# Kernel optimization log

Hardware: AMD Instinct MI355X
Metric: run time of the kernel (lower is better)

The kernel has to match this reference:

```python
import jax, jax.numpy as jnp
import numpy as np

THRESHOLD = 0.5


def setup_inputs() -> dict:
    key = jax.random.key(0)
    T, B = 2048, 4096
    x = jax.random.uniform(key, (T, B, 2), dtype=jnp.float32)  # push/pop signals in [0,1]
    state0 = jnp.zeros((B, 2), dtype=jnp.float32)  # [count, tanh(count)]
    return {"x": x, "state0": state0}


def _step(state, xt):
    # state: [B, 2] = [count, tanh(count)]; xt: [B, 2] = [push, pop]
    push_sig = xt[..., 0]
    pop_sig = xt[..., 1]
    is_push = (push_sig >= THRESHOLD) & (push_sig >= pop_sig)
    is_pop = (pop_sig >= THRESHOLD) & (pop_sig > push_sig)
    delta = jnp.where(is_push, 1.0, jnp.where(is_pop, -1.0, 0.0))
    count = state[..., 0] + delta
    new_state = jnp.stack([count, jnp.tanh(count)], axis=-1)
    return new_state, new_state


def reference(x, state0):
    # x: [T, B, 2], state0: [B, 2] -> all per-step states [T, B, 2]
    _, states = jax.lax.scan(_step, state0, x)
    return states
```

## Files before the change

kernel.cpp:

```cpp
#include <hip/hip_runtime.h>
#include <math.h>

#define T_TOTAL 2048
#define B_TOTAL 4096
#define NCHUNK  32
#define TCHUNK  (T_TOTAL / NCHUNK)

__device__ __forceinline__ int delta_of(float p, float q) {
    return (p >= 0.5f && p >= q) ? 1 : ((q >= 0.5f && q > p) ? -1 : 0);
}

__global__ void scan_pass1(const float* __restrict__ x, int* __restrict__ partial) {
    const int b = blockIdx.x * blockDim.x + threadIdx.x;
    const int c = blockIdx.y;
    const float2* __restrict__ x2 = (const float2*)x;
    const int t0 = c * TCHUNK;
    int sum = 0;
#pragma unroll 4
    for (int t = t0; t < t0 + TCHUNK; ++t) {
        float2 v = x2[(size_t)t * B_TOTAL + b];
        sum += delta_of(v.x, v.y);
    }
    partial[c * B_TOTAL + b] = sum;
}

__global__ void scan_pass2(int* __restrict__ partial) {
    const int b = blockIdx.x * blockDim.x + threadIdx.x;
    int off = 0;
#pragma unroll
    for (int c = 0; c < NCHUNK; ++c) {
        int v = partial[c * B_TOTAL + b];
        partial[c * B_TOTAL + b] = off;
        off += v;
    }
}

__global__ void scan_pass3(const float* __restrict__ x, const int* __restrict__ partial,
                           float* __restrict__ out) {
    const int b = blockIdx.x * blockDim.x + threadIdx.x;
    const int c = blockIdx.y;
    const float2* __restrict__ x2 = (const float2*)x;
    float2* __restrict__ o2 = (float2*)out;
    const int t0 = c * TCHUNK;
    int count = partial[c * B_TOTAL + b];
#pragma unroll 4
    for (int t = t0; t < t0 + TCHUNK; ++t) {
        float2 v = x2[(size_t)t * B_TOTAL + b];
        count += delta_of(v.x, v.y);
        float fc = (float)count;
        float2 w;
        w.x = fc;
        w.y = tanhf(fc);
        o2[(size_t)t * B_TOTAL + b] = w;
    }
}

__global__ void naive_scan(const float* __restrict__ x, float* __restrict__ out) {
    const int b = blockIdx.x * blockDim.x + threadIdx.x;
    if (b >= B_TOTAL) return;
    const float2* __restrict__ x2 = (const float2*)x;
    float2* __restrict__ o2 = (float2*)out;
    int count = 0;
    for (int t = 0; t < T_TOTAL; ++t) {
        float2 v = x2[(size_t)t * B_TOTAL + b];
        count += delta_of(v.x, v.y);
        float fc = (float)count;
        float2 w;
        w.x = fc;
        w.y = tanhf(fc);
        o2[(size_t)t * B_TOTAL + b] = w;
    }
}

extern "C" void kernel_launch(void* const* d_in, const int* in_sizes, int n_in,
                              void* d_out, int out_size, void* d_ws, size_t ws_size,
                              hipStream_t stream) {
    const float* x = (const float*)d_in[0];
    float* out = (float*)d_out;

    const size_t partial_bytes = (size_t)NCHUNK * B_TOTAL * sizeof(int);
    if (ws_size < partial_bytes) {
        naive_scan<<<dim3((B_TOTAL + 255) / 256), dim3(256), 0, stream>>>(x, out);
        return;
    }
    int* partial = (int*)d_ws;

    dim3 block(256);
    dim3 grid1(B_TOTAL / 256, NCHUNK);
    scan_pass1<<<grid1, block, 0, stream>>>(x, partial);
    scan_pass2<<<dim3(B_TOTAL / 256), block, 0, stream>>>(partial);
    scan_pass3<<<grid1, block, 0, stream>>>(x, partial, out);
}
```

Baseline: 134.0 us.

## Pack per-step deltas in pass1 so pass3 skips rereading input

Pass 1 now encodes each step's push/pop delta as 2 bits and writes them to a packed workspace buffer. Pass 3 decodes those bits instead of reading the 64MB input a second time. Each thread handles two batch lanes through float4 loads and stores, the chunk count doubles to 64, and tanhf is replaced by an exp2-based fast approximation. The aim is to remove one full read of the input. The cost is extra workspace, and the fast tanh may be slightly less accurate.

```diff
diff --git a/kernel.cpp b/kernel.cpp
--- a/kernel.cpp
+++ b/kernel.cpp
@@ -3,25 +3,53 @@
 
 #define T_TOTAL 2048
 #define B_TOTAL 4096
-#define NCHUNK  32
+#define B2      (B_TOTAL / 2)
+#define NCHUNK  64
 #define TCHUNK  (T_TOTAL / NCHUNK)
 
 __device__ __forceinline__ int delta_of(float p, float q) {
     return (p >= 0.5f && p >= q) ? 1 : ((q >= 0.5f && q > p) ? -1 : 0);
 }
 
-__global__ void scan_pass1(const float* __restrict__ x, int* __restrict__ partial) {
-    const int b = blockIdx.x * blockDim.x + threadIdx.x;
+__device__ __forceinline__ float fast_tanh(float x) {
+    float e = __builtin_amdgcn_exp2f(x * 2.885390081777927f);
+    return 1.0f - 2.0f / (e + 1.0f);
+}
+
+__global__ void scan_pass1(const float* __restrict__ x,
+                           int* __restrict__ partial,
+                           ulonglong2* __restrict__ packed) {
+    const int p = blockIdx.x * blockDim.x + threadIdx.x;
     const int c = blockIdx.y;
-    const float2* __restrict__ x2 = (const float2*)x;
+    const float4* __restrict__ x4 = (const float4*)x;
     const int t0 = c * TCHUNK;
-    int sum = 0;
-#pragma unroll 4
-    for (int t = t0; t < t0 + TCHUNK; ++t) {
-        float2 v = x2[(size_t)t * B_TOTAL + b];
-        sum += delta_of(v.x, v.y);
+
+    int s0 = 0, s1 = 0;
+    unsigned long long w0 = 0ull, w1 = 0ull;
+
+#pragma unroll
+    for (int t = 0; t < 16; ++t) {
+        float4 v = x4[(size_t)(t0 + t) * B2 + p];
+        int d0 = delta_of(v.x, v.y);
+        int d1 = delta_of(v.z, v.w);
+        s0 += d0; s1 += d1;
+        unsigned int nib = (unsigned int)(d0 & 3) | ((unsigned int)(d1 & 3) << 2);
+        w0 |= (unsigned long long)nib << (4 * t);
     }
-    partial[c * B_TOTAL + b] = sum;
+#pragma unroll
+    for (int t = 16; t < 32; ++t) {
+        float4 v = x4[(size_t)(t0 + t) * B2 + p];
+        int d0 = delta_of(v.x, v.y);
+        int d1 = delta_of(v.z, v.w);
+        s0 += d0; s1 += d1;
+        unsigned int nib = (unsigned int)(d0 & 3) | ((unsigned int)(d1 & 3) << 2);
+        w1 |= (unsigned long long)nib << (4 * (t - 16));
+    }
+
+    ulonglong2 w; w.x = w0; w.y = w1;
+    packed[(size_t)c * B2 + p] = w;
+    int2 s; s.x = s0; s.y = s1;
+    ((int2*)partial)[(size_t)c * B2 + p] = s;
 }
 
 __global__ void scan_pass2(int* __restrict__ partial) {
@@ -29,29 +57,45 @@
     int off = 0;
 #pragma unroll
     for (int c = 0; c < NCHUNK; ++c) {
-        int v = partial[c * B_TOTAL + b];
-        partial[c * B_TOTAL + b] = off;
+        int v = partial[(size_t)c * B_TOTAL + b];
+        partial[(size_t)c * B_TOTAL + b] = off;
         off += v;
     }
 }
 
-__global__ void scan_pass3(const float* __restrict__ x, const int* __restrict__ partial,
+__device__ __forceinline__ int sext2(unsigned int bits2) {
+    return ((int)(bits2 << 30)) >> 30;
+}
+
+__global__ void scan_pass3(const int* __restrict__ partial,
+                           const ulonglong2* __restrict__ packed,
                            float* __restrict__ out) {
-    const int b = blockIdx.x * blockDim.x + threadIdx.x;
+    const int p = blockIdx.x * blockDim.x + threadIdx.x;
     const int c = blockIdx.y;
-    const float2* __restrict__ x2 = (const float2*)x;
-    float2* __restrict__ o2 = (float2*)out;
+    float4* __restrict__ o4 = (float4*)out;
     const int t0 = c * TCHUNK;
-    int count = partial[c * B_TOTAL + b];
-#pragma unroll 4
-    for (int t = t0; t < t0 + TCHUNK; ++t) {
-        float2 v = x2[(size_t)t * B_TOTAL + b];
-        count += delta_of(v.x, v.y);
-        float fc = (float)count;
-        float2 w;
-        w.x = fc;
-        w.y = tanhf(fc);
-        o2[(size_t)t * B_TOTAL + b] = w;
+
+    int2 pr = ((const int2*)partial)[(size_t)c * B2 + p];
+    int c0 = pr.x, c1 = pr.y;
+    ulonglong2 w = packed[(size_t)c * B2 + p];
+
+#pragma unroll
+    for (int t = 0; t < 16; ++t) {
+        unsigned int nib = (unsigned int)(w.x >> (4 * t)) & 0xFu;
+        c0 += sext2(nib & 3u);
+        c1 += sext2(nib >> 2);
+        float f0 = (float)c0, f1 = (float)c1;
+        float4 o; o.x = f0; o.y = fast_tanh(f0); o.z = f1; o.w = fast_tanh(f1);
+        o4[(size_t)(t0 + t) * B2 + p] = o;
+    }
+#pragma unroll
+    for (int t = 16; t < 32; ++t) {
+        unsigned int nib = (unsigned int)(w.y >> (4 * (t - 16))) & 0xFu;
+        c0 += sext2(nib & 3u);
+        c1 += sext2(nib >> 2);
+        float f0 = (float)c0, f1 = (float)c1;
+        float4 o; o.x = f0; o.y = fast_tanh(f0); o.z = f1; o.w = fast_tanh(f1);
+        o4[(size_t)(t0 + t) * B2 + p] = o;
     }
 }
 
@@ -65,9 +109,7 @@
         float2 v = x2[(size_t)t * B_TOTAL + b];
         count += delta_of(v.x, v.y);
         float fc = (float)count;
-        float2 w;
-        w.x = fc;
-        w.y = tanhf(fc);
+        float2 w; w.x = fc; w.y = tanhf(fc);
         o2[(size_t)t * B_TOTAL + b] = w;
     }
 }
@@ -79,15 +121,17 @@
     float* out = (float*)d_out;
 
     const size_t partial_bytes = (size_t)NCHUNK * B_TOTAL * sizeof(int);
-    if (ws_size < partial_bytes) {
+    const size_t packed_bytes  = (size_t)NCHUNK * B2 * sizeof(ulonglong2);
+    if (ws_size < partial_bytes + packed_bytes) {
         naive_scan<<<dim3((B_TOTAL + 255) / 256), dim3(256), 0, stream>>>(x, out);
         return;
     }
     int* partial = (int*)d_ws;
+    ulonglong2* packed = (ulonglong2*)((char*)d_ws + partial_bytes);
 
     dim3 block(256);
-    dim3 grid1(B_TOTAL / 256, NCHUNK);
-    scan_pass1<<<grid1, block, 0, stream>>>(x, partial);
+    dim3 grid1(B2 / 256, NCHUNK);
+    scan_pass1<<<grid1, block, 0, stream>>>(x, partial, packed);
     scan_pass2<<<dim3(B_TOTAL / 256), block, 0, stream>>>(partial);
-    scan_pass3<<<grid1, block, 0, stream>>>(x, partial, out);
+    scan_pass3<<<grid1, block, 0, stream>>>(partial, packed, out);
 }
```

New measurement: 115.5 us. -13.8%, faster.
